# Kernel optimization log

Hardware: AMD Instinct MI355X
Metric: run time of the kernel (lower is better)

Reference implementation:

```python
import jax, jax.numpy as jnp
import numpy as np
from functools import partial

# dims matching init_kwargs
H = 512      # hidden_size
F = 2048     # ff_size
NH = 8       # num_heads
NL = 6       # num_layers
V = 1024     # vocab_size
T = 8        # sentence_length
S = 5        # n_sentences_in_paragraph
P = 16       # n_paragraphs_in_article
L = P * S * T          # article_length = 640
N = L + 1              # sequence length used by masks = 641
B = 16                 # batch
HD = H // NH           # head dim
LN_EPS = 1e-5
NEG = -1e9


def _build_mask():
    # pseudo_causal_masks[0] from the torch __init__: causal ~tril plus
    # blocking of within-paragraph sentence-0 key columns.
    a = np.ones((P, S, T, P, S, T), dtype=bool)
    j = np.arange(P)
    a[j, :, :, j, 0, :] = False
    a = a.reshape(L, L)
    causal = ~np.tril(np.ones((N, N), dtype=bool))
    m = causal.copy()
    m[:-1, 1:] = np.logical_and(a, causal[:-1, 1:])
    return m  # True = disallowed


def _build_pe():
    # sinusoidal pe exactly as in __init__ (div_term uses hidden_size in denom)
    pos = np.arange(N, dtype=np.float32)[:, None]
    div = np.exp(np.arange(0, H // 2, dtype=np.float32) * (-np.log(10000.0) / H))
    pe = np.zeros((N, H), dtype=np.float32)
    pe[:, 0::2] = np.sin(pos * div)
    pe[:, 1::2] = np.cos(pos * div)
    return pe


def setup_inputs() -> dict:
    key = jax.random.key(0)
    ks = jax.random.split(key, 12)
    sd = 0.02
    inp = {
        'tokens': jax.random.randint(ks[0], (B, N), 0, V),
        'attn_mask': jnp.asarray(_build_mask()),
        'pe': jnp.asarray(_build_pe()),
        'emb': jax.random.normal(ks[1], (V, H), jnp.float32) * sd,
        'qkv_w': jax.random.normal(ks[2], (NL, 3 * H, H), jnp.float32) * sd,
        'qkv_b': jnp.zeros((NL, 3 * H), jnp.float32),
        'out_w': jax.random.normal(ks[3], (NL, H, H), jnp.float32) * sd,
        'out_b': jnp.zeros((NL, H), jnp.float32),
        'ln1_g': jnp.ones((NL, H), jnp.float32),
        'ln1_b': jnp.zeros((NL, H), jnp.float32),
        'fc1_w': jax.random.normal(ks[4], (NL, F, H), jnp.float32) * sd,
        'fc1_b': jnp.zeros((NL, F), jnp.float32),
        'fc2_w': jax.random.normal(ks[5], (NL, H, F), jnp.float32) * sd,
        'fc2_b': jnp.zeros((NL, H), jnp.float32),
        'ln2_g': jnp.ones((NL, H), jnp.float32),
        'ln2_b': jnp.zeros((NL, H), jnp.float32),
        'lnf_g': jnp.ones((H,), jnp.float32),
        'lnf_b': jnp.zeros((H,), jnp.float32),
        'dep_w': jax.random.normal(ks[6], (V, H), jnp.float32) * sd,
        'dep_b': jnp.zeros((V,), jnp.float32),
    }
    return inp


def _ln(x, g, b):
    m = jnp.mean(x, axis=-1, keepdims=True)
    v = jnp.mean(jnp.square(x - m), axis=-1, keepdims=True)
    return (x - m) * jax.lax.rsqrt(v + LN_EPS) * g + b


def _encoder_layer(x, p, mask):
    qw, qb, ow, ob, g1, b1, w1, bb1, w2, bb2, g2, b2 = p
    Bsz, Nn, _ = x.shape
    qkv = x @ qw.T + qb                                   # [B,N,3H]
    q, k, v = jnp.split(qkv, 3, axis=-1)
    q = q.reshape(Bsz, Nn, NH, HD)
    k = k.reshape(Bsz, Nn, NH, HD)
    v = v.reshape(Bsz, Nn, NH, HD)
    scores = jnp.einsum('bqhd,bkhd->bhqk', q, k) / jnp.sqrt(jnp.asarray(HD, x.dtype))
    scores = jnp.where(mask[None, None], NEG, scores)
    att = jax.nn.softmax(scores, axis=-1)
    o = jnp.einsum('bhqk,bkhd->bqhd', att, v).reshape(Bsz, Nn, H)
    o = o @ ow.T + ob
    x = _ln(x + o, g1, b1)                                # post-LN (torch default)
    f = jax.nn.gelu(x @ w1.T + bb1, approximate=False) @ w2.T + bb2
    return _ln(x + f, g2, b2)


def reference(tokens, attn_mask, pe, emb, qkv_w, qkv_b, out_w, out_b,
              ln1_g, ln1_b, fc1_w, fc1_b, fc2_w, fc2_b, ln2_g, ln2_b,
              lnf_g, lnf_b, dep_w, dep_b):
    x = emb[tokens] + pe[None]                            # [B,N,H]
    layers = (qkv_w, qkv_b, out_w, out_b, ln1_g, ln1_b,
              fc1_w, fc1_b, fc2_w, fc2_b, ln2_g, ln2_b)

    def step(h, p):
        return _encoder_layer(h, p, attn_mask), None

    x, _ = jax.lax.scan(step, x, layers)
    x = _ln(x, lnf_g, lnf_b)
    return x @ dep_w.T + dep_b                            # [B,N,V] logits
```

## Files before the change

### kernel.cpp

```cpp
#include <hip/hip_runtime.h>
#include <stdint.h>

#define NSEQ 641
#define BATCH 16
#define MROWS (BATCH * NSEQ)
#define HID 512
#define FFD 2048
#define NHEAD 8
#define HDIM 64
#define NLAYER 6
#define VOCAB 1024
#define KPAD 704

typedef __bf16 bf16x8 __attribute__((ext_vector_type(8)));
typedef float  f32x4  __attribute__((ext_vector_type(4)));
typedef int    i32x4  __attribute__((ext_vector_type(4)));
typedef short  s16x8  __attribute__((ext_vector_type(8)));
typedef short  s16x4  __attribute__((ext_vector_type(4)));

#define EXP_C 0.18033688011112042f

__device__ __forceinline__ uint32_t swz(uint32_t b) { return b ^ (((b >> 7) & 7u) << 4); }
__device__ __forceinline__ uint32_t swz32(uint32_t b) { return b ^ (((b >> 7) & 3u) << 4); }

__device__ __forceinline__ int xcd_swz(int bid, int nwg) {
  int x = bid & 7, j = bid >> 3;
  int q = nwg >> 3, r = nwg & 7;
  return x * q + (x < r ? x : r) + j;
}

__device__ __forceinline__ unsigned short f2bf(float f) {
  uint32_t u = __builtin_bit_cast(uint32_t, f);
  u += 0x7FFFu + ((u >> 16) & 1u);
  return (unsigned short)(u >> 16);
}

__device__ __forceinline__ void gload16(const void* g, void* l) {
  __builtin_amdgcn_global_load_lds(
      (const __attribute__((address_space(1))) uint32_t*)g,
      (__attribute__((address_space(3))) uint32_t*)l, 16, 0, 0);
}

__device__ __forceinline__ bf16x8 ld_lds16(const void* p) {
  return __builtin_bit_cast(bf16x8, *(const i32x4*)p);
}

__global__ void cvt_kernel(const float* __restrict__ in,
                           unsigned short* __restrict__ out, int n) {
  int i = (blockIdx.x * 256 + threadIdx.x) * 4;
  if (i >= n) return;
  f32x4 v = *(const f32x4*)(in + i);
  s16x4 o;
  o[0] = (short)f2bf(v[0]); o[1] = (short)f2bf(v[1]);
  o[2] = (short)f2bf(v[2]); o[3] = (short)f2bf(v[3]);
  *(s16x4*)(out + i) = o;
}

__global__ void embed_kernel(const int* __restrict__ tok,
                             const float* __restrict__ emb,
                             const float* __restrict__ pe,
                             float* __restrict__ x,
                             unsigned short* __restrict__ xb) {
  int m = blockIdx.x;
  int n = m % NSEQ;
  int t = tok[m];
  int h = threadIdx.x * 4;
  f32x4 e = *(const f32x4*)(emb + (size_t)t * HID + h);
  f32x4 p = *(const f32x4*)(pe + (size_t)n * HID + h);
  f32x4 v = e + p;
  *(f32x4*)(x + (size_t)m * HID + h) = v;
  s16x4 o;
  o[0] = (short)f2bf(v[0]); o[1] = (short)f2bf(v[1]);
  o[2] = (short)f2bf(v[2]); o[3] = (short)f2bf(v[3]);
  *(s16x4*)(xb + (size_t)m * HID + h) = o;
}

__global__ __launch_bounds__(256) void ln_kernel(
    const float* __restrict__ in, const float* __restrict__ gg,
    const float* __restrict__ bb, float* __restrict__ xo,
    unsigned short* __restrict__ xbo, int rows) {
  int row = blockIdx.x * 4 + (threadIdx.x >> 6);
  if (row >= rows) return;
  int lane = threadIdx.x & 63;
  const float* p = in + (size_t)row * HID + lane * 8;
  f32x4 a0 = *(const f32x4*)p;
  f32x4 a1 = *(const f32x4*)(p + 4);
  float s = a0[0] + a0[1] + a0[2] + a0[3] + a1[0] + a1[1] + a1[2] + a1[3];
#pragma unroll
  for (int o = 32; o; o >>= 1) s += __shfl_xor(s, o);
  float mean = s * (1.0f / HID);
  float vs = 0.f;
#pragma unroll
  for (int j = 0; j < 4; ++j) { float d = a0[j] - mean; vs += d * d; }
#pragma unroll
  for (int j = 0; j < 4; ++j) { float d = a1[j] - mean; vs += d * d; }
#pragma unroll
  for (int o = 32; o; o >>= 1) vs += __shfl_xor(vs, o);
  float rstd = rsqrtf(vs * (1.0f / HID) + 1e-5f);
  f32x4 g0 = *(const f32x4*)(gg + lane * 8);
  f32x4 g1 = *(const f32x4*)(gg + lane * 8 + 4);
  f32x4 b0 = *(const f32x4*)(bb + lane * 8);
  f32x4 b1 = *(const f32x4*)(bb + lane * 8 + 4);
  f32x4 y0, y1;
  s16x8 ob;
#pragma unroll
  for (int j = 0; j < 4; ++j) {
    y0[j] = (a0[j] - mean) * rstd * g0[j] + b0[j];
    y1[j] = (a1[j] - mean) * rstd * g1[j] + b1[j];
    ob[j] = (short)f2bf(y0[j]);
    ob[j + 4] = (short)f2bf(y1[j]);
  }
  float* xp = xo + (size_t)row * HID + lane * 8;
  *(f32x4*)xp = y0;
  *(f32x4*)(xp + 4) = y1;
  *(s16x8*)(xbo + (size_t)row * HID + lane * 8) = ob;
}

__global__ __launch_bounds__(256) void vtrans_kernel(
    const unsigned short* __restrict__ V, unsigned short* __restrict__ vT) {
  const int kt = blockIdx.x;
  const int bh = blockIdx.y;
  const int k0 = kt * 64;
  const int tid = threadIdx.x;
  __shared__ unsigned short lds[64][68];
  const size_t src = (size_t)bh * (NSEQ * HDIM);
#pragma unroll
  for (int it = 0; it < 2; ++it) {
    int k = it * 32 + (tid >> 3);
    int d0 = (tid & 7) * 8;
    int kr = k0 + k;
    s16x8 v = {};
    if (kr < NSEQ) v = *(const s16x8*)(V + src + (size_t)kr * HDIM + d0);
    *(s16x8*)&lds[k][d0] = v;
  }
  __syncthreads();
  const int d = tid & 63;
  const int w = tid >> 6;
  const size_t dst = ((size_t)bh * 64 + d) * KPAD + k0;
#pragma unroll
  for (int it = 0; it < 2; ++it) {
    int kc = w + it * 4;
    s16x8 o;
#pragma unroll
    for (int i = 0; i < 8; ++i) o[i] = lds[kc * 8 + i][d];
    *(s16x8*)(vT + dst + kc * 8) = o;
  }
}

enum { EPI_QKV = 0, EPI_GELU = 1, EPI_RESID = 2, EPI_F32OUT = 3 };

template <int EPI>
__global__ __launch_bounds__(256, 3) void gemm_bt(
    const unsigned short* __restrict__ A, const unsigned short* __restrict__ W,
    const float* __restrict__ bias, const float* __restrict__ resid,
    void* __restrict__ out0, void* __restrict__ out1, void* __restrict__ out2,
    int M, int N, int K) {
  __shared__ char sm[3][16384];
  const int tid = threadIdx.x, lane = tid & 63, wid = tid >> 6;
  const int wr = wid >> 1, wc = wid & 1;
  const int lg = lane >> 4, lc = lane & 15;

  const int nx = N >> 7;
  const int logical = xcd_swz(blockIdx.x, gridDim.x);
  const int m0 = (logical / nx) * 128, n0 = (logical % nx) * 128;

  f32x4 acc[4][4] = {};

  auto stage = [&](int kt, char* dst) {
#pragma unroll
    for (int i = 0; i < 2; ++i) {
      uint32_t P = (uint32_t)tid * 16 + i * 4096;
      uint32_t L = swz32(P);
      int row = (int)(L >> 6);
      uint32_t kb = L & 63u;
      int ma = m0 + row; if (ma >= M) ma = M - 1;
      gload16((const char*)A + ((size_t)ma * K + kt) * 2 + kb, dst + P);
      gload16((const char*)W + ((size_t)(n0 + row) * K + kt) * 2 + kb,
              dst + 8192 + P);
    }
  };

  const int nk = K >> 5;
  stage(0, sm[0]);
  stage(32, sm[1]);

  int bc = 0;
  for (int t = 0; t < nk; ++t) {
    if (t + 1 < nk) asm volatile("s_waitcnt vmcnt(4)" ::: "memory");
    else            asm volatile("s_waitcnt vmcnt(0)" ::: "memory");
    __builtin_amdgcn_sched_barrier(0);
    __builtin_amdgcn_s_barrier();
    __builtin_amdgcn_sched_barrier(0);
    if (t + 2 < nk) {
      int b2 = bc + 2; if (b2 >= 3) b2 -= 3;
      stage((t + 2) << 5, sm[b2]);
    }
    const char* buf = sm[bc];
    bf16x8 af[4], bfr[4];
#pragma unroll
    for (int mi = 0; mi < 4; ++mi) {
      int row = wr * 64 + mi * 16 + lc;
      af[mi] = ld_lds16(buf + swz32((uint32_t)row * 64 + (lg << 4)));
    }
#pragma unroll
    for (int ni = 0; ni < 4; ++ni) {
      int row = wc * 64 + ni * 16 + lc;
      bfr[ni] = ld_lds16(buf + 8192 + swz32((uint32_t)row * 64 + (lg << 4)));
    }
#pragma unroll
    for (int mi = 0; mi < 4; ++mi)
#pragma unroll
      for (int ni = 0; ni < 4; ++ni)
        acc[mi][ni] = __builtin_amdgcn_mfma_f32_16x16x32_bf16(af[mi], bfr[ni], acc[mi][ni], 0, 0, 0);
    asm volatile("s_waitcnt lgkmcnt(0)" ::: "memory");
    __builtin_amdgcn_sched_barrier(0);
    if (++bc == 3) bc = 0;
  }

#pragma unroll
  for (int mi = 0; mi < 4; ++mi) {
#pragma unroll
    for (int g = 0; g < 4; ++g) {
      int m = m0 + wr * 64 + mi * 16 + lg * 4 + g;
      if (m >= M) continue;
      int bbq = 0, nn = 0;
      if (EPI == EPI_QKV) { bbq = m / NSEQ; nn = m - bbq * NSEQ; }
#pragma unroll
      for (int ni = 0; ni < 4; ++ni) {
        int c = n0 + wc * 64 + ni * 16 + lc;
        float v = acc[mi][ni][g] + bias[c];
        if (EPI == EPI_QKV) {
          int which = c >> 9, hh = (c >> 6) & 7, d = c & 63;
          unsigned short* dst = which == 0 ? (unsigned short*)out0
                              : which == 1 ? (unsigned short*)out1
                                           : (unsigned short*)out2;
          dst[(((size_t)bbq * NHEAD + hh) * NSEQ + nn) * HDIM + d] = f2bf(v);
        } else if (EPI == EPI_GELU) {
          v = 0.5f * v * (1.0f + erff(v * 0.70710678118654752f));
          ((unsigned short*)out0)[(size_t)m * N + c] = f2bf(v);
        } else if (EPI == EPI_RESID) {
          float* o = (float*)out0;
          o[(size_t)m * N + c] = v + resid[(size_t)m * N + c];
        } else {
          ((float*)out0)[(size_t)m * N + c] = v;
        }
      }
    }
  }
}

__global__ __launch_bounds__(256) void attn_kernel(
    const unsigned short* __restrict__ Q, const unsigned short* __restrict__ Kb,
    const unsigned short* __restrict__ vT, unsigned short* __restrict__ O) {
  const int logical = xcd_swz(blockIdx.x, gridDim.x);
  const int qt = logical % 11, bh = logical / 11;
  const int b = bh >> 3, h = bh & 7;
  const int q0 = qt * 64;
  const int tid = threadIdx.x, lane = tid & 63, w = tid >> 6;
  const int lg = lane >> 4, lc = lane & 15;
  __shared__ char sK[2][8192];
  __shared__ char sV[2][8192];
  __shared__ char sP[4][2048];

  const size_t base = (size_t)bh * (NSEQ * HDIM);
  const size_t baseT = (size_t)bh * (HDIM * KPAD);

  bf16x8 qf[2];
  {
    int qr = q0 + w * 16 + lc;
    if (qr > NSEQ - 1) qr = NSEQ - 1;
#pragma unroll
    for (int kk = 0; kk < 2; ++kk)
      qf[kk] = __builtin_bit_cast(
          bf16x8, *(const i32x4*)(Q + base + (size_t)qr * HDIM + kk * 32 + (lg << 3)));
  }

  f32x4 acc[4] = {};
  float lsum[4] = {0.f, 0.f, 0.f, 0.f};
  const int qrow_base = q0 + w * 16 + (lg << 2);

  int nkt = qt + 2;
  if (nkt > 11) nkt = 11;

  auto stage = [&](int kt, int bufi) {
    const int k0 = kt * 64;
#pragma unroll
    for (int i = 0; i < 2; ++i) {
      uint32_t P = w * 2048 + i * 1024 + lane * 16;
      uint32_t L = swz(P);
      int row = (int)(L >> 7);
      uint32_t kbyte = L & 127u;
      int kr = k0 + row; if (kr > NSEQ - 1) kr = NSEQ - 1;
      gload16((const char*)(Kb + base + (size_t)kr * HDIM) + kbyte,
              sK[bufi] + w * 2048 + i * 1024);
      gload16((const char*)(vT + baseT + (size_t)row * KPAD + k0) + kbyte,
              sV[bufi] + w * 2048 + i * 1024);
    }
  };

  stage(0, 0);
  __syncthreads();

  for (int kt = 0; kt < nkt; ++kt) {
    if (kt + 1 < nkt) stage(kt + 1, (kt + 1) & 1);
    const char* bK = sK[kt & 1];
    const char* bV = sV[kt & 1];
    const int k0 = kt * 64;

    f32x4 s[4] = {};
#pragma unroll
    for (int nt = 0; nt < 4; ++nt) {
#pragma unroll
      for (int kk = 0; kk < 2; ++kk) {
        int row = nt * 16 + lc;
        bf16x8 kf = ld_lds16(bK + swz((uint32_t)row * 128 + kk * 64 + (lg << 4)));
        s[nt] = __builtin_amdgcn_mfma_f32_16x16x32_bf16(qf[kk], kf, s[nt], 0, 0, 0);
      }
    }

    if (kt < qt) {
#pragma unroll
      for (int g = 0; g < 4; ++g)
#pragma unroll
        for (int nt = 0; nt < 4; ++nt) {
          float p = exp2f(s[nt][g] * EXP_C);
          s[nt][g] = p;
          lsum[g] += p;
        }
    } else if (kt == qt) {
#pragma unroll
      for (int g = 0; g < 4; ++g) {
        int q = qrow_base + g;
        int pp = q / 40;
        int lo = pp * 40 + 1, hi = pp * 40 + 8;
#pragma unroll
        for (int nt = 0; nt < 4; ++nt) {
          int k = k0 + nt * 16 + lc;
          bool ok = ((k <= q) || (k >= lo && k <= hi)) && (k < NSEQ);
          float p = ok ? exp2f(s[nt][g] * EXP_C) : 0.f;
          s[nt][g] = p;
          lsum[g] += p;
        }
      }
    } else {
#pragma unroll
      for (int g = 0; g < 4; ++g) {
        int q = qrow_base + g;
        int pp = q / 40;
        int lo = pp * 40 + 1, hi = pp * 40 + 8;
#pragma unroll
        for (int nt = 0; nt < 4; ++nt) {
          int k = k0 + nt * 16 + lc;
          bool ok = (k >= lo && k <= hi) && (k < NSEQ);
          float p = ok ? exp2f(s[nt][g] * EXP_C) : 0.f;
          s[nt][g] = p;
          lsum[g] += p;
        }
      }
    }

#pragma unroll
    for (int g = 0; g < 4; ++g) {
      int row = (lg << 2) + g;
#pragma unroll
      for (int nt = 0; nt < 4; ++nt) {
        int col = nt * 16 + lc;
        *(short*)(sP[w] + swz((uint32_t)row * 128 + col * 2)) = (short)f2bf(s[nt][g]);
      }
    }
#pragma unroll
    for (int kk = 0; kk < 2; ++kk) {
      bf16x8 pa = ld_lds16(sP[w] + swz((uint32_t)lc * 128 + kk * 64 + (lg << 4)));
#pragma unroll
      for (int nt = 0; nt < 4; ++nt) {
        int rowv = nt * 16 + lc;
        bf16x8 vf = ld_lds16(bV + swz((uint32_t)rowv * 128 + kk * 64 + (lg << 4)));
        acc[nt] = __builtin_amdgcn_mfma_f32_16x16x32_bf16(pa, vf, acc[nt], 0, 0, 0);
      }
    }
    __syncthreads();
  }

#pragma unroll
  for (int o = 1; o < 16; o <<= 1)
#pragma unroll
    for (int g = 0; g < 4; ++g) lsum[g] += __shfl_xor(lsum[g], o);

#pragma unroll
  for (int g = 0; g < 4; ++g) {
    int q = qrow_base + g;
    if (q >= NSEQ) continue;
    float inv = 1.0f / lsum[g];
#pragma unroll
    for (int nt = 0; nt < 4; ++nt) {
      int d = nt * 16 + lc;
      O[((size_t)b * NSEQ + q) * HID + h * HDIM + d] = f2bf(acc[nt][g] * inv);
    }
  }
}

extern "C" void kernel_launch(void* const* d_in, const int* in_sizes, int n_in,
                              void* d_out, int out_size, void* d_ws, size_t ws_size,
                              hipStream_t stream) {
  const int*   tok   = (const int*)d_in[0];
  const float* pe    = (const float*)d_in[2];
  const float* emb   = (const float*)d_in[3];
  const float* qkv_w = (const float*)d_in[4];
  const float* qkv_b = (const float*)d_in[5];
  const float* out_w = (const float*)d_in[6];
  const float* out_b = (const float*)d_in[7];
  const float* ln1_g = (const float*)d_in[8];
  const float* ln1_b = (const float*)d_in[9];
  const float* fc1_w = (const float*)d_in[10];
  const float* fc1_b = (const float*)d_in[11];
  const float* fc2_w = (const float*)d_in[12];
  const float* fc2_b = (const float*)d_in[13];
  const float* ln2_g = (const float*)d_in[14];
  const float* ln2_b = (const float*)d_in[15];
  const float* lnf_g = (const float*)d_in[16];
  const float* lnf_b = (const float*)d_in[17];
  const float* dep_w = (const float*)d_in[18];
  const float* dep_b = (const float*)d_in[19];

  const size_t SZ_QKV = (size_t)1536 * 512;
  const size_t SZ_OUT = (size_t)512 * 512;
  const size_t SZ_FC1 = (size_t)2048 * 512;
  const size_t SZ_FC2 = (size_t)512 * 2048;
  const size_t SZ_DEP = (size_t)VOCAB * 512;

  char* w = (char*)d_ws;
  float* x = (float*)w;            w += (size_t)MROWS * HID * 4;
  unsigned short* xb = (unsigned short*)w; w += (size_t)MROWS * HID * 2;
  unsigned short* qb = (unsigned short*)w; w += (size_t)BATCH * NHEAD * NSEQ * HDIM * 2;
  unsigned short* kb = (unsigned short*)w; w += (size_t)BATCH * NHEAD * NSEQ * HDIM * 2;
  unsigned short* vb = (unsigned short*)w; w += (size_t)BATCH * NHEAD * NSEQ * HDIM * 2;
  unsigned short* ao = (unsigned short*)w; w += (size_t)BATCH * NHEAD * NSEQ * HDIM * 2;
  unsigned short* mid = qb;
  unsigned short* vT = (unsigned short*)w; w += (size_t)BATCH * NHEAD * HDIM * KPAD * 2;

  size_t used = (size_t)(w - (char*)d_ws);
  size_t all_w_bytes = (NLAYER * (SZ_QKV + SZ_OUT + SZ_FC1 + SZ_FC2) + SZ_DEP) * 2;
  bool upfront = ws_size >= used + all_w_bytes;

  unsigned short *wq_all, *wo_all, *w1_all, *w2_all, *wd;
  if (upfront) {
    wq_all = (unsigned short*)w; w += NLAYER * SZ_QKV * 2;
    wo_all = (unsigned short*)w; w += NLAYER * SZ_OUT * 2;
    w1_all = (unsigned short*)w; w += NLAYER * SZ_FC1 * 2;
    w2_all = (unsigned short*)w; w += NLAYER * SZ_FC2 * 2;
    wd     = (unsigned short*)w; w += SZ_DEP * 2;
    cvt_kernel<<<dim3((NLAYER * SZ_QKV) / 1024), 256, 0, stream>>>(qkv_w, wq_all, NLAYER * SZ_QKV);
    cvt_kernel<<<dim3((NLAYER * SZ_OUT) / 1024), 256, 0, stream>>>(out_w, wo_all, NLAYER * SZ_OUT);
    cvt_kernel<<<dim3((NLAYER * SZ_FC1) / 1024), 256, 0, stream>>>(fc1_w, w1_all, NLAYER * SZ_FC1);
    cvt_kernel<<<dim3((NLAYER * SZ_FC2) / 1024), 256, 0, stream>>>(fc2_w, w2_all, NLAYER * SZ_FC2);
    cvt_kernel<<<dim3(SZ_DEP / 1024), 256, 0, stream>>>(dep_w, wd, SZ_DEP);
  } else {
    wq_all = (unsigned short*)w; w += SZ_QKV * 2;
    wo_all = (unsigned short*)w; w += SZ_OUT * 2;
    w1_all = (unsigned short*)w; w += SZ_FC1 * 2;
    w2_all = (unsigned short*)w; w += SZ_FC2 * 2;
    wd     = (unsigned short*)w; w += SZ_DEP * 2;
    cvt_kernel<<<dim3(SZ_DEP / 1024), 256, 0, stream>>>(dep_w, wd, SZ_DEP);
  }

  embed_kernel<<<dim3(MROWS), 128, 0, stream>>>(tok, emb, pe, x, xb);

  const int lnBlocks = (MROWS + 3) / 4;
  for (int l = 0; l < NLAYER; ++l) {
    unsigned short *wq, *wo, *w1, *w2;
    if (upfront) {
      wq = wq_all + l * SZ_QKV; wo = wo_all + l * SZ_OUT;
      w1 = w1_all + l * SZ_FC1; w2 = w2_all + l * SZ_FC2;
    } else {
      wq = wq_all; wo = wo_all; w1 = w1_all; w2 = w2_all;
      cvt_kernel<<<dim3(SZ_QKV / 1024), 256, 0, stream>>>(qkv_w + l * SZ_QKV, wq, SZ_QKV);
      cvt_kernel<<<dim3(SZ_OUT / 1024), 256, 0, stream>>>(out_w + l * SZ_OUT, wo, SZ_OUT);
      cvt_kernel<<<dim3(SZ_FC1 / 1024), 256, 0, stream>>>(fc1_w + l * SZ_FC1, w1, SZ_FC1);
      cvt_kernel<<<dim3(SZ_FC2 / 1024), 256, 0, stream>>>(fc2_w + l * SZ_FC2, w2, SZ_FC2);
    }

    gemm_bt<EPI_QKV><<<dim3(12 * 81), 256, 0, stream>>>(
        xb, wq, qkv_b + l * 1536, nullptr, qb, kb, vb, MROWS, 1536, 512);
    vtrans_kernel<<<dim3(11, 128), 256, 0, stream>>>(vb, vT);
    attn_kernel<<<dim3(11 * 128), 256, 0, stream>>>(qb, kb, vT, ao);
    gemm_bt<EPI_RESID><<<dim3(4 * 81), 256, 0, stream>>>(
        ao, wo, out_b + l * 512, x, x, nullptr, nullptr, MROWS, 512, 512);
    ln_kernel<<<dim3(lnBlocks), 256, 0, stream>>>(x, ln1_g + l * 512, ln1_b + l * 512, x, xb, MROWS);
    gemm_bt<EPI_GELU><<<dim3(16 * 81), 256, 0, stream>>>(
        xb, w1, fc1_b + l * 2048, nullptr, mid, nullptr, nullptr, MROWS, 2048, 512);
    gemm_bt<EPI_RESID><<<dim3(4 * 81), 256, 0, stream>>>(
        mid, w2, fc2_b + l * 512, x, x, nullptr, nullptr, MROWS, 512, 2048);
    ln_kernel<<<dim3(lnBlocks), 256, 0, stream>>>(x, ln2_g + l * 512, ln2_b + l * 512, x, xb, MROWS);
  }

  ln_kernel<<<dim3(lnBlocks), 256, 0, stream>>>(x, lnf_g, lnf_b, x, xb, MROWS);
  gemm_bt<EPI_F32OUT><<<dim3(8 * 81), 256, 0, stream>>>(
      xb, wd, dep_b, nullptr, d_out, nullptr, nullptr, MROWS, VOCAB, 512);
}
```

Before: 1.395 ms.

## Add BM=64 GEMM tiles for narrow GEMMs and 128-row attention query tiles

The GEMM is templated on its M tile size. The N=512 and vocab GEMMs now use 64-row tiles, doubling their grid, which addresses too few blocks (324) on a many-CU device. The attention kernel now processes 128 query rows per block, each wave handling two 16-row fragments. This reuses each staged K/V tile across twice as many queries and halves the number of blocks. The cost is more registers per attention block, fewer attention blocks overall, and slightly more masked tiles per block.

After: 1.510 ms. 8.3% more time.

```diff
diff --git a/kernel.cpp b/kernel.cpp
--- a/kernel.cpp
+++ b/kernel.cpp
@@ -149,34 +149,46 @@
 
 enum { EPI_QKV = 0, EPI_GELU = 1, EPI_RESID = 2, EPI_F32OUT = 3 };
 
-template <int EPI>
+template <int EPI, int BM>
 __global__ __launch_bounds__(256, 3) void gemm_bt(
     const unsigned short* __restrict__ A, const unsigned short* __restrict__ W,
     const float* __restrict__ bias, const float* __restrict__ resid,
     void* __restrict__ out0, void* __restrict__ out1, void* __restrict__ out2,
     int M, int N, int K) {
-  __shared__ char sm[3][16384];
+  constexpr int ASZ = BM * 64;
+  constexpr int BUF = ASZ + 8192;
+  constexpr int MI = BM >> 5;
+  constexpr int WROWS = BM >> 1;
+  constexpr int ALOADS = ASZ / 4096;
+  __shared__ char sm[3][BUF];
   const int tid = threadIdx.x, lane = tid & 63, wid = tid >> 6;
   const int wr = wid >> 1, wc = wid & 1;
   const int lg = lane >> 4, lc = lane & 15;
 
   const int nx = N >> 7;
   const int logical = xcd_swz(blockIdx.x, gridDim.x);
-  const int m0 = (logical / nx) * 128, n0 = (logical % nx) * 128;
-
-  f32x4 acc[4][4] = {};
+  const int m0 = (logical / nx) * BM, n0 = (logical % nx) * 128;
+
+  f32x4 acc[MI][4] = {};
 
   auto stage = [&](int kt, char* dst) {
 #pragma unroll
-    for (int i = 0; i < 2; ++i) {
+    for (int i = 0; i < ALOADS; ++i) {
       uint32_t P = (uint32_t)tid * 16 + i * 4096;
       uint32_t L = swz32(P);
       int row = (int)(L >> 6);
       uint32_t kb = L & 63u;
       int ma = m0 + row; if (ma >= M) ma = M - 1;
       gload16((const char*)A + ((size_t)ma * K + kt) * 2 + kb, dst + P);
+    }
+#pragma unroll
+    for (int i = 0; i < 2; ++i) {
+      uint32_t P = (uint32_t)tid * 16 + i * 4096;
+      uint32_t L = swz32(P);
+      int row = (int)(L >> 6);
+      uint32_t kb = L & 63u;
       gload16((const char*)W + ((size_t)(n0 + row) * K + kt) * 2 + kb,
-              dst + 8192 + P);
+              dst + ASZ + P);
     }
   };
 
@@ -186,8 +198,12 @@
 
   int bc = 0;
   for (int t = 0; t < nk; ++t) {
-    if (t + 1 < nk) asm volatile("s_waitcnt vmcnt(4)" ::: "memory");
-    else            asm volatile("s_waitcnt vmcnt(0)" ::: "memory");
+    if (t + 1 < nk) {
+      if constexpr (ALOADS == 2) asm volatile("s_waitcnt vmcnt(4)" ::: "memory");
+      else                       asm volatile("s_waitcnt vmcnt(3)" ::: "memory");
+    } else {
+      asm volatile("s_waitcnt vmcnt(0)" ::: "memory");
+    }
     __builtin_amdgcn_sched_barrier(0);
     __builtin_amdgcn_s_barrier();
     __builtin_amdgcn_sched_barrier(0);
@@ -196,19 +212,19 @@
       stage((t + 2) << 5, sm[b2]);
     }
     const char* buf = sm[bc];
-    bf16x8 af[4], bfr[4];
-#pragma unroll
-    for (int mi = 0; mi < 4; ++mi) {
-      int row = wr * 64 + mi * 16 + lc;
+    bf16x8 af[MI], bfr[4];
+#pragma unroll
+    for (int mi = 0; mi < MI; ++mi) {
+      int row = wr * WROWS + mi * 16 + lc;
       af[mi] = ld_lds16(buf + swz32((uint32_t)row * 64 + (lg << 4)));
     }
 #pragma unroll
     for (int ni = 0; ni < 4; ++ni) {
       int row = wc * 64 + ni * 16 + lc;
-      bfr[ni] = ld_lds16(buf + 8192 + swz32((uint32_t)row * 64 + (lg << 4)));
-    }
-#pragma unroll
-    for (int mi = 0; mi < 4; ++mi)
+      bfr[ni] = ld_lds16(buf + ASZ + swz32((uint32_t)row * 64 + (lg << 4)));
+    }
+#pragma unroll
+    for (int mi = 0; mi < MI; ++mi)
 #pragma unroll
       for (int ni = 0; ni < 4; ++ni)
         acc[mi][ni] = __builtin_amdgcn_mfma_f32_16x16x32_bf16(af[mi], bfr[ni], acc[mi][ni], 0, 0, 0);
@@ -218,10 +234,10 @@
   }
 
 #pragma unroll
-  for (int mi = 0; mi < 4; ++mi) {
+  for (int mi = 0; mi < MI; ++mi) {
 #pragma unroll
     for (int g = 0; g < 4; ++g) {
-      int m = m0 + wr * 64 + mi * 16 + lg * 4 + g;
+      int m = m0 + wr * WROWS + mi * 16 + lg * 4 + g;
       if (m >= M) continue;
       int bbq = 0, nn = 0;
       if (EPI == EPI_QKV) { bbq = m / NSEQ; nn = m - bbq * NSEQ; }
@@ -253,33 +269,33 @@
     const unsigned short* __restrict__ Q, const unsigned short* __restrict__ Kb,
     const unsigned short* __restrict__ vT, unsigned short* __restrict__ O) {
   const int logical = xcd_swz(blockIdx.x, gridDim.x);
-  const int qt = logical % 11, bh = logical / 11;
+  const int qt = logical % 6, bh = logical / 6;
   const int b = bh >> 3, h = bh & 7;
-  const int q0 = qt * 64;
+  const int q0 = qt * 128;
   const int tid = threadIdx.x, lane = tid & 63, w = tid >> 6;
   const int lg = lane >> 4, lc = lane & 15;
   __shared__ char sK[2][8192];
   __shared__ char sV[2][8192];
-  __shared__ char sP[4][2048];
+  __shared__ char sP[4][4096];
 
   const size_t base = (size_t)bh * (NSEQ * HDIM);
   const size_t baseT = (size_t)bh * (HDIM * KPAD);
 
-  bf16x8 qf[2];
-  {
-    int qr = q0 + w * 16 + lc;
+  bf16x8 qf[2][2];
+#pragma unroll
+  for (int fr = 0; fr < 2; ++fr) {
+    int qr = q0 + w * 32 + fr * 16 + lc;
     if (qr > NSEQ - 1) qr = NSEQ - 1;
 #pragma unroll
     for (int kk = 0; kk < 2; ++kk)
-      qf[kk] = __builtin_bit_cast(
+      qf[fr][kk] = __builtin_bit_cast(
           bf16x8, *(const i32x4*)(Q + base + (size_t)qr * HDIM + kk * 32 + (lg << 3)));
   }
 
-  f32x4 acc[4] = {};
-  float lsum[4] = {0.f, 0.f, 0.f, 0.f};
-  const int qrow_base = q0 + w * 16 + (lg << 2);
-
-  int nkt = qt + 2;
+  f32x4 acc[2][4] = {};
+  float lsum[2][4] = {};
+
+  int nkt = 2 * qt + 3;
   if (nkt > 11) nkt = 11;
 
   auto stage = [&](int kt, int bufi) {
@@ -306,97 +322,92 @@
     const char* bK = sK[kt & 1];
     const char* bV = sV[kt & 1];
     const int k0 = kt * 64;
-
-    f32x4 s[4] = {};
-#pragma unroll
-    for (int nt = 0; nt < 4; ++nt) {
-#pragma unroll
-      for (int kk = 0; kk < 2; ++kk) {
-        int row = nt * 16 + lc;
-        bf16x8 kf = ld_lds16(bK + swz((uint32_t)row * 128 + kk * 64 + (lg << 4)));
-        s[nt] = __builtin_amdgcn_mfma_f32_16x16x32_bf16(qf[kk], kf, s[nt], 0, 0, 0);
-      }
-    }
-
-    if (kt < qt) {
-#pragma unroll
-      for (int g = 0; g < 4; ++g)
-#pragma unroll
-        for (int nt = 0; nt < 4; ++nt) {
-          float p = exp2f(s[nt][g] * EXP_C);
-          s[nt][g] = p;
-          lsum[g] += p;
-        }
-    } else if (kt == qt) {
-#pragma unroll
-      for (int g = 0; g < 4; ++g) {
-        int q = qrow_base + g;
-        int pp = q / 40;
-        int lo = pp * 40 + 1, hi = pp * 40 + 8;
-#pragma unroll
-        for (int nt = 0; nt < 4; ++nt) {
-          int k = k0 + nt * 16 + lc;
-          bool ok = ((k <= q) || (k >= lo && k <= hi)) && (k < NSEQ);
-          float p = ok ? exp2f(s[nt][g] * EXP_C) : 0.f;
-          s[nt][g] = p;
-          lsum[g] += p;
+    const bool allowed_all = (kt < 2 * qt);
+
+#pragma unroll
+    for (int fr = 0; fr < 2; ++fr) {
+      f32x4 s[4] = {};
+#pragma unroll
+      for (int nt = 0; nt < 4; ++nt) {
+#pragma unroll
+        for (int kk = 0; kk < 2; ++kk) {
+          int row = nt * 16 + lc;
+          bf16x8 kf = ld_lds16(bK + swz((uint32_t)row * 128 + kk * 64 + (lg << 4)));
+          s[nt] = __builtin_amdgcn_mfma_f32_16x16x32_bf16(qf[fr][kk], kf, s[nt], 0, 0, 0);
         }
       }
-    } else {
-#pragma unroll
-      for (int g = 0; g < 4; ++g) {
-        int q = qrow_base + g;
-        int pp = q / 40;
-        int lo = pp * 40 + 1, hi = pp * 40 + 8;
-#pragma unroll
-        for (int nt = 0; nt < 4; ++nt) {
-          int k = k0 + nt * 16 + lc;
-          bool ok = (k >= lo && k <= hi) && (k < NSEQ);
-          float p = ok ? exp2f(s[nt][g] * EXP_C) : 0.f;
-          s[nt][g] = p;
-          lsum[g] += p;
+      if (allowed_all) {
+#pragma unroll
+        for (int g = 0; g < 4; ++g)
+#pragma unroll
+          for (int nt = 0; nt < 4; ++nt) {
+            float p = exp2f(s[nt][g] * EXP_C);
+            s[nt][g] = p;
+            lsum[fr][g] += p;
+          }
+      } else {
+#pragma unroll
+        for (int g = 0; g < 4; ++g) {
+          int q = q0 + w * 32 + fr * 16 + (lg << 2) + g;
+          int pp = q / 40;
+          int lo = pp * 40 + 1, hi = pp * 40 + 8;
+#pragma unroll
+          for (int nt = 0; nt < 4; ++nt) {
+            int k = k0 + nt * 16 + lc;
+            bool ok = ((k <= q) || (k >= lo && k <= hi)) && (k < NSEQ);
+            float p = ok ? exp2f(s[nt][g] * EXP_C) : 0.f;
+            s[nt][g] = p;
+            lsum[fr][g] += p;
+          }
         }
       }
-    }
-
+#pragma unroll
+      for (int g = 0; g < 4; ++g) {
+        int row = fr * 16 + (lg << 2) + g;
+#pragma unroll
+        for (int nt = 0; nt < 4; ++nt) {
+          int col = nt * 16 + lc;
+          *(short*)(sP[w] + swz((uint32_t)row * 128 + col * 2)) = (short)f2bf(s[nt][g]);
+        }
+      }
+    }
+#pragma unroll
+    for (int fr = 0; fr < 2; ++fr) {
+#pragma unroll
+      for (int kk = 0; kk < 2; ++kk) {
+        int rowp = fr * 16 + lc;
+        bf16x8 pa = ld_lds16(sP[w] + swz((uint32_t)rowp * 128 + kk * 64 + (lg << 4)));
+#pragma unroll
+        for (int nt = 0; nt < 4; ++nt) {
+          int rowv = nt * 16 + lc;
+          bf16x8 vf = ld_lds16(bV + swz((uint32_t)rowv * 128 + kk * 64 + (lg << 4)));
+          acc[fr][nt] = __builtin_amdgcn_mfma_f32_16x16x32_bf16(pa, vf, acc[fr][nt], 0, 0, 0);
+        }
+      }
+    }
+    __syncthreads();
+  }
+
+#pragma unroll
+  for (int o = 1; o < 16; o <<= 1)
+#pragma unroll
+    for (int fr = 0; fr < 2; ++fr)
+#pragma unroll
+      for (int g = 0; g < 4; ++g) lsum[fr][g] += __shfl_xor(lsum[fr][g], o);
+
+#pragma unroll
+  for (int fr = 0; fr < 2; ++fr)
 #pragma unroll
     for (int g = 0; g < 4; ++g) {
-      int row = (lg << 2) + g;
+      int q = q0 + w * 32 + fr * 16 + (lg << 2) + g;
+      if (q >= NSEQ) continue;
+      float inv = 1.0f / lsum[fr][g];
 #pragma unroll
       for (int nt = 0; nt < 4; ++nt) {
-        int col = nt * 16 + lc;
-        *(short*)(sP[w] + swz((uint32_t)row * 128 + col * 2)) = (short)f2bf(s[nt][g]);
+        int d = nt * 16 + lc;
+        O[((size_t)b * NSEQ + q) * HID + h * HDIM + d] = f2bf(acc[fr][nt][g] * inv);
       }
     }
-#pragma unroll
-    for (int kk = 0; kk < 2; ++kk) {
-      bf16x8 pa = ld_lds16(sP[w] + swz((uint32_t)lc * 128 + kk * 64 + (lg << 4)));
-#pragma unroll
-      for (int nt = 0; nt < 4; ++nt) {
-        int rowv = nt * 16 + lc;
-        bf16x8 vf = ld_lds16(bV + swz((uint32_t)rowv * 128 + kk * 64 + (lg << 4)));
-        acc[nt] = __builtin_amdgcn_mfma_f32_16x16x32_bf16(pa, vf, acc[nt], 0, 0, 0);
-      }
-    }
-    __syncthreads();
-  }
-
-#pragma unroll
-  for (int o = 1; o < 16; o <<= 1)
-#pragma unroll
-    for (int g = 0; g < 4; ++g) lsum[g] += __shfl_xor(lsum[g], o);
-
-#pragma unroll
-  for (int g = 0; g < 4; ++g) {
-    int q = qrow_base + g;
-    if (q >= NSEQ) continue;
-    float inv = 1.0f / lsum[g];
-#pragma unroll
-    for (int nt = 0; nt < 4; ++nt) {
-      int d = nt * 16 + lc;
-      O[((size_t)b * NSEQ + q) * HID + h * HDIM + d] = f2bf(acc[nt][g] * inv);
-    }
-  }
 }
 
 extern "C" void kernel_launch(void* const* d_in, const int* in_sizes, int n_in,
@@ -479,21 +490,21 @@
       cvt_kernel<<<dim3(SZ_FC2 / 1024), 256, 0, stream>>>(fc2_w + l * SZ_FC2, w2, SZ_FC2);
     }
 
-    gemm_bt<EPI_QKV><<<dim3(12 * 81), 256, 0, stream>>>(
+    gemm_bt<EPI_QKV, 128><<<dim3(12 * 81), 256, 0, stream>>>(
         xb, wq, qkv_b + l * 1536, nullptr, qb, kb, vb, MROWS, 1536, 512);
     vtrans_kernel<<<dim3(11, 128), 256, 0, stream>>>(vb, vT);
-    attn_kernel<<<dim3(11 * 128), 256, 0, stream>>>(qb, kb, vT, ao);
-    gemm_bt<EPI_RESID><<<dim3(4 * 81), 256, 0, stream>>>(
+    attn_kernel<<<dim3(6 * 128), 256, 0, stream>>>(qb, kb, vT, ao);
+    gemm_bt<EPI_RESID, 64><<<dim3(4 * 161), 256, 0, stream>>>(
         ao, wo, out_b + l * 512, x, x, nullptr, nullptr, MROWS, 512, 512);
     ln_kernel<<<dim3(lnBlocks), 256, 0, stream>>>(x, ln1_g + l * 512, ln1_b + l * 512, x, xb, MROWS);
-    gemm_bt<EPI_GELU><<<dim3(16 * 81), 256, 0, stream>>>(
+    gemm_bt<EPI_GELU, 128><<<dim3(16 * 81), 256, 0, stream>>>(
         xb, w1, fc1_b + l * 2048, nullptr, mid, nullptr, nullptr, MROWS, 2048, 512);
-    gemm_bt<EPI_RESID><<<dim3(4 * 81), 256, 0, stream>>>(
+    gemm_bt<EPI_RESID, 64><<<dim3(4 * 161), 256, 0, stream>>>(
         mid, w2, fc2_b + l * 512, x, x, nullptr, nullptr, MROWS, 512, 2048);
     ln_kernel<<<dim3(lnBlocks), 256, 0, stream>>>(x, ln2_g + l * 512, ln2_b + l * 512, x, xb, MROWS);
   }
 
   ln_kernel<<<dim3(lnBlocks), 256, 0, stream>>>(x, lnf_g, lnf_b, x, xb, MROWS);
-  gemm_bt<EPI_F32OUT><<<dim3(8 * 81), 256, 0, stream>>>(
+  gemm_bt<EPI_F32OUT, 64><<<dim3(8 * 161), 256, 0, stream>>>(
       xb, wd, dep_b, nullptr, d_out, nullptr, nullptr, MROWS, VOCAB, 512);
 }
```
